# Kernel optimization log

Measured on AMD Instinct MI355X. Metric: run time of the kernel, lower is better.

## Reference

```python
import jax, jax.numpy as jnp
import numpy as np

N, D, H, K = 131072, 512, 128, 3
NPOS, NNEG = 8192, 8192
KM_ITERS = 4
PROTO_SHIFT = 0.15
PROTO_LOGIT_SCALE = 0.2
TEMP = 2.5


def _sq_cdist(x, c):
    # squared euclidean distance, matches torch.cdist(...).pow(2)
    d = jnp.sum(x * x, -1, keepdims=True) + jnp.sum(c * c, -1)[None, :] - 2.0 * (x @ c.T)
    return jnp.maximum(d, 0.0)


def _kmeans(x, k, iters):
    # torch.linspace(0, n-1, steps=k).long() init, fixed iteration count
    n = x.shape[0]
    idx = jnp.linspace(0.0, n - 1, k).astype(jnp.int32)
    centers = x[idx]
    for _ in range(iters):
        assign = jnp.argmin(_sq_cdist(x, centers), axis=1)
        sums = jax.ops.segment_sum(x, assign, num_segments=k)
        counts = jax.ops.segment_sum(jnp.ones((n,), x.dtype), assign, num_segments=k)[:, None]
        # empty cluster keeps old center (mask.any() branch in torch)
        centers = jnp.where(counts > 0, sums / jnp.maximum(counts, 1.0), centers)
    return centers


def setup_inputs() -> dict:
    key = jax.random.key(0)
    ks = jax.random.split(key, 10)
    s = 1.0 / np.sqrt(D).astype(np.float32)
    return {
        "z_cls": jax.random.normal(ks[0], (N, D), jnp.float32),
        "z_proto": jax.random.normal(ks[1], (N, D), jnp.float32),
        "pos_ctx": jax.random.normal(ks[2], (D,), jnp.float32),
        "neg_ctx": jax.random.normal(ks[3], (D,), jnp.float32),
        "W1": jax.random.normal(ks[4], (H, D), jnp.float32) * s,
        "b1": jnp.zeros((H,), jnp.float32),
        "W2": jax.random.normal(ks[5], (1, H), jnp.float32) * (1.0 / np.sqrt(H).astype(np.float32)),
        "b2": jnp.zeros((1,), jnp.float32),
        "Wp": jax.random.normal(ks[6], (D, D), jnp.float32) * s,
        "bp": jnp.zeros((D,), jnp.float32),
        "Wn": jax.random.normal(ks[7], (D, D), jnp.float32) * s,
        "bn": jnp.zeros((D,), jnp.float32),
        "pos_idx": jax.random.randint(ks[8], (NPOS,), 0, N),
        "neg_idx": jax.random.randint(ks[9], (NNEG,), 0, N),
    }


def reference(z_cls, z_proto, pos_ctx, neg_ctx, W1, b1, W2, b2, Wp, bp, Wn, bn, pos_idx, neg_idx):
    # _build_prototypes (pos_idx/neg_idx nonempty path)
    pos_proto = _kmeans(z_proto[pos_idx], K, KM_ITERS)          # [K, D]
    neg_proto = jnp.mean(z_proto[neg_idx], axis=0)              # [D]
    # _calibrate (ema not initialized -> no EMA blend)
    pos_proto = pos_proto + PROTO_SHIFT * (pos_ctx @ Wp.T + bp)[None, :]
    neg_proto = neg_proto + PROTO_SHIFT * (neg_ctx @ Wn.T + bn)
    # distances
    d_pos_all = _sq_cdist(z_proto, pos_proto)                   # [N, K]
    d_pos = jnp.min(d_pos_all, axis=1)
    pos_assign = jnp.argmin(d_pos_all, axis=1)
    d_neg = jnp.mean((z_proto - neg_proto[None, :]) ** 2, axis=1)
    proto_logit = (d_neg - d_pos) / np.sqrt(D).astype(np.float32)
    # cls head (eval mode: dropout is identity)
    h = jax.nn.relu(z_cls @ W1.T + b1)
    cls_logit = (h @ W2.T + b2)[:, 0]
    logits = (cls_logit + PROTO_LOGIT_SCALE * proto_logit) / TEMP
    prob = jax.nn.sigmoid(logits)
    return (logits, prob, PROTO_LOGIT_SCALE * proto_logit, pos_assign, d_pos_all, pos_proto, neg_proto)
```

## Files before the change

### kernel.cpp

```cpp
#include <hip/hip_runtime.h>
#include <hip/hip_bf16.h>

#define NPTS 131072
#define DIM  512
#define HID  128
#define KCL  3
#define NPOSI 8192
#define NNEGI 8192

typedef __attribute__((ext_vector_type(8))) short bf16x8;
typedef __attribute__((ext_vector_type(4))) float f32x4;

enum {
  WS_SHIFT_POS = 0,
  WS_SHIFT_NEG = 512,
  WS_NEGSUM    = 1024,
  WS_NEGPART   = 1536,
  WS_SUMS      = 67072,
  WS_W1FRAG    = 73232,
};
#define SUMS_STRIDE 1539

__device__ __forceinline__ short f2bf(float x) {
  __hip_bfloat16 h = __float2bfloat16(x);
  return *reinterpret_cast<short*>(&h);
}

__global__ __launch_bounds__(256) void k_prep(const float* __restrict__ W1,
                                              const float* __restrict__ Wp, const float* __restrict__ bp,
                                              const float* __restrict__ Wn, const float* __restrict__ bn,
                                              const float* __restrict__ pos_ctx, const float* __restrict__ neg_ctx,
                                              const float* __restrict__ zp, const int* __restrict__ neg_idx,
                                              float* __restrict__ ws) {
  int bid = blockIdx.x, t = threadIdx.x;
  if (bid < 32) {
    int fid = bid * 256 + t;
    int kc = fid >> 9;
    int n  = (fid >> 6) & 7;
    int l  = fid & 63;
    int row = n * 16 + (l & 15);
    int col = kc * 32 + (l >> 4) * 8;
    const float* src = W1 + (size_t)row * DIM + col;
    float4 v0 = *(const float4*)(src);
    float4 v1 = *(const float4*)(src + 4);
    bf16x8 f;
    f[0] = f2bf(v0.x); f[1] = f2bf(v0.y); f[2] = f2bf(v0.z); f[3] = f2bf(v0.w);
    f[4] = f2bf(v1.x); f[5] = f2bf(v1.y); f[6] = f2bf(v1.z); f[7] = f2bf(v1.w);
    ((bf16x8*)(ws + WS_W1FRAG))[fid] = f;
  } else if (bid < 64) {
    int b = bid - 32;
    int mat = b >> 4;
    const float* W    = mat ? Wn : Wp;
    const float* bias = mat ? bn : bp;
    const float* ctx  = mat ? neg_ctx : pos_ctx;
    float* outp = ws + (mat ? WS_SHIFT_NEG : WS_SHIFT_POS);
    int row = (b & 15) * 32 + (t >> 3);
    int sub = t & 7;
    const float* wr = W + row * DIM + sub * 64;
    const float* cr = ctx + sub * 64;
    float s = 0.f;
#pragma unroll
    for (int j = 0; j < 64; j += 4) {
      float4 w4 = *(const float4*)(wr + j);
      float4 c4 = *(const float4*)(cr + j);
      s += w4.x * c4.x + w4.y * c4.y + w4.z * c4.z + w4.w * c4.w;
    }
    s += __shfl_xor(s, 1);
    s += __shfl_xor(s, 2);
    s += __shfl_xor(s, 4);
    if (sub == 0) outp[row] = 0.15f * (s + bias[row]);
  } else if (bid < 192) {
    int j = bid - 64;
    int c0 = t * 2;
    float a0 = 0.f, a1 = 0.f;
    int j0 = j * 64;
    for (int jj = 0; jj < 64; ++jj) {
      int row = neg_idx[j0 + jj];
      float2 v = *(const float2*)(zp + (size_t)row * DIM + c0);
      a0 += v.x; a1 += v.y;
    }
    ws[WS_NEGPART + j * DIM + c0]     = a0;
    ws[WS_NEGPART + j * DIM + c0 + 1] = a1;
  } else {
    for (int idx = t; idx < 4 * SUMS_STRIDE; idx += 256) ws[WS_SUMS + idx] = 0.f;
  }
}

template <int IT>
__global__ __launch_bounds__(256) void k_km(const float* __restrict__ zp,
                                            const int* __restrict__ pos_idx,
                                            float* __restrict__ ws) {
  int bid = blockIdx.x, t = threadIdx.x;
  if (IT == 0 && bid == 256) {
    int c0 = t * 2;
    float a0 = 0.f, a1 = 0.f;
#pragma unroll 8
    for (int j = 0; j < 128; ++j) {
      float2 v = *(const float2*)(ws + WS_NEGPART + j * DIM + c0);
      a0 += v.x; a1 += v.y;
    }
    ws[WS_NEGSUM + c0]     = a0;
    ws[WS_NEGSUM + c0 + 1] = a1;
    return;
  }
  __shared__ float cc[KCL * DIM];
  __shared__ float cn[KCL];
  __shared__ float lsum[KCL * DIM];
  __shared__ float lcnt[KCL];
  int w = t >> 6, l = t & 63;

  for (int idx = t; idx < KCL * DIM; idx += 256) lsum[idx] = 0.f;
  if (t < KCL) lcnt[t] = 0.f;

  for (int idx = t; idx < KCL * DIM; idx += 256) {
    int k = idx >> 9;
    int sel = (k == 0) ? 0 : ((k == 1) ? 4095 : 8191);
    float v = zp[(size_t)pos_idx[sel] * DIM + (idx & 511)];
#pragma unroll
    for (int j = 0; j < IT; ++j) {
      float cntv = ws[WS_SUMS + j * SUMS_STRIDE + 3 * DIM + k];
      float sv   = ws[WS_SUMS + j * SUMS_STRIDE + idx];
      v = (cntv > 0.f) ? sv / cntv : v;
    }
    cc[idx] = v;
  }
  __syncthreads();
  if (w < KCL) {
    float s = 0.f;
#pragma unroll
    for (int m = 0; m < 8; ++m) { float v = cc[w * DIM + l + m * 64]; s += v * v; }
#pragma unroll
    for (int m = 1; m < 64; m <<= 1) s += __shfl_xor(s, m);
    if (l == 0) cn[w] = s;
  }
  __syncthreads();

  float ck0[8], ck1[8], ck2[8];
#pragma unroll
  for (int j = 0; j < 8; ++j) {
    ck0[j] = cc[0 * DIM + l * 8 + j];
    ck1[j] = cc[1 * DIM + l * 8 + j];
    ck2[j] = cc[2 * DIM + l * 8 + j];
  }
  float cn0 = cn[0], cn1 = cn[1], cn2 = cn[2];
  float acc0[8] = {0,0,0,0,0,0,0,0}, acc1[8] = {0,0,0,0,0,0,0,0}, acc2[8] = {0,0,0,0,0,0,0,0};
  float cnt0 = 0.f, cnt1 = 0.f, cnt2 = 0.f;

  int wid = bid * 4 + w;
  for (int p = wid; p < NPOSI; p += 1024) {
    int row = pos_idx[p];
    const float* xr = zp + (size_t)row * DIM + l * 8;
    float4 x0 = *(const float4*)(xr);
    float4 x1 = *(const float4*)(xr + 4);
    float x[8] = {x0.x, x0.y, x0.z, x0.w, x1.x, x1.y, x1.z, x1.w};
    float d0 = 0.f, d1 = 0.f, d2 = 0.f;
#pragma unroll
    for (int j = 0; j < 8; ++j) { d0 += x[j] * ck0[j]; d1 += x[j] * ck1[j]; d2 += x[j] * ck2[j]; }
#pragma unroll
    for (int m = 1; m < 64; m <<= 1) {
      d0 += __shfl_xor(d0, m); d1 += __shfl_xor(d1, m); d2 += __shfl_xor(d2, m);
    }
    float t0 = cn0 - 2.f * d0, t1 = cn1 - 2.f * d1, t2 = cn2 - 2.f * d2;
    int a = 0; float best = t0;
    if (t1 < best) { best = t1; a = 1; }
    if (t2 < best) { best = t2; a = 2; }
    if (a == 0)      { cnt0 += 1.f;
#pragma unroll
      for (int j = 0; j < 8; ++j) acc0[j] += x[j]; }
    else if (a == 1) { cnt1 += 1.f;
#pragma unroll
      for (int j = 0; j < 8; ++j) acc1[j] += x[j]; }
    else             { cnt2 += 1.f;
#pragma unroll
      for (int j = 0; j < 8; ++j) acc2[j] += x[j]; }
  }
#pragma unroll
  for (int j = 0; j < 8; ++j) {
    atomicAdd(&lsum[0 * DIM + l * 8 + j], acc0[j]);
    atomicAdd(&lsum[1 * DIM + l * 8 + j], acc1[j]);
    atomicAdd(&lsum[2 * DIM + l * 8 + j], acc2[j]);
  }
  if (l == 0) {
    atomicAdd(&lcnt[0], cnt0); atomicAdd(&lcnt[1], cnt1); atomicAdd(&lcnt[2], cnt2);
  }
  __syncthreads();
  for (int idx = t; idx < KCL * DIM; idx += 256) atomicAdd(&ws[WS_SUMS + IT * SUMS_STRIDE + idx], lsum[idx]);
  if (t < KCL) atomicAdd(&ws[WS_SUMS + IT * SUMS_STRIDE + 3 * DIM + t], lcnt[t]);
}

__global__ __launch_bounds__(256) void k_main(const float* __restrict__ zc,
                                              const float* __restrict__ zp,
                                              const float* __restrict__ b1,
                                              const float* __restrict__ W2,
                                              const float* __restrict__ b2,
                                              const int* __restrict__ pos_idx,
                                              const float* __restrict__ ws,
                                              float* __restrict__ out) {
  __shared__ float pp[KCL * DIM];
  __shared__ float np[DIM];
  __shared__ float pn[4];
  __shared__ float clsv[64];
  __shared__ float sxs[64];
  __shared__ float dstg[4][64];
  __shared__ float outst[448];
  __shared__ bf16x8 pfrag[1024];

  int t = threadIdx.x, w = t >> 6, l = t & 63;
  int i0 = blockIdx.x * 64;

  for (int idx = t; idx < KCL * DIM; idx += 256) {
    int k = idx >> 9, d = idx & 511;
    int sel = (k == 0) ? 0 : ((k == 1) ? 4095 : 8191);
    float v = zp[(size_t)pos_idx[sel] * DIM + d];
#pragma unroll
    for (int j = 0; j < 4; ++j) {
      float cntv = ws[WS_SUMS + j * SUMS_STRIDE + 3 * DIM + k];
      float sv   = ws[WS_SUMS + j * SUMS_STRIDE + idx];
      v = (cntv > 0.f) ? sv / cntv : v;
    }
    pp[idx] = v + ws[WS_SHIFT_POS + d];
  }
  for (int d = t; d < DIM; d += 256)
    np[d] = ws[WS_NEGSUM + d] * (1.f / NNEGI) + ws[WS_SHIFT_NEG + d];
  __syncthreads();
  {
    float s = 0.f;
    const float* src = (w < 3) ? (pp + w * DIM) : np;
#pragma unroll
    for (int m = 0; m < 8; ++m) { float v = src[l + m * 64]; s += v * v; }
#pragma unroll
    for (int m = 1; m < 64; m <<= 1) s += __shfl_xor(s, m);
    if (l == 0) pn[w] = s;
  }
  for (int idx = t; idx < 1024; idx += 256) {
    int kc = idx >> 6, ll = idx & 63, c = ll & 15, ko = (ll >> 4) * 8;
    bf16x8 v;
#pragma unroll
    for (int j = 0; j < 8; ++j) {
      float f = (c < 3) ? pp[c * DIM + kc * 32 + ko + j]
                        : ((c == 3) ? np[kc * 32 + ko + j] : 0.f);
      v[j] = f2bf(f);
    }
    pfrag[idx] = v;
  }
  if (blockIdx.x == 0) {
    for (int idx = t; idx < KCL * DIM; idx += 256) out[7 * NPTS + idx] = pp[idx];
    for (int d = t; d < DIM; d += 256)            out[7 * NPTS + KCL * DIM + d] = np[d];
  }
  __syncthreads();

  const bf16x8* w1f = (const bf16x8*)(ws + WS_W1FRAG);
  int arow = i0 + w * 16 + (l & 15);
  const float* zcrow = zc + (size_t)arow * DIM + (l >> 4) * 8;
  const float* zprow = zp + (size_t)arow * DIM + (l >> 4) * 8;

  f32x4 accc[8];
#pragma unroll
  for (int n = 0; n < 8; ++n) accc[n] = (f32x4){0.f, 0.f, 0.f, 0.f};
  f32x4 accd = (f32x4){0.f, 0.f, 0.f, 0.f};
  float sx = 0.f;

  for (int kc = 0; kc < 16; ++kc) {
    float4 c0 = *(const float4*)(zcrow + kc * 32);
    float4 c1 = *(const float4*)(zcrow + kc * 32 + 4);
    float4 p0 = *(const float4*)(zprow + kc * 32);
    float4 p1 = *(const float4*)(zprow + kc * 32 + 4);
    bf16x8 af, ap;
    af[0] = f2bf(c0.x); af[1] = f2bf(c0.y); af[2] = f2bf(c0.z); af[3] = f2bf(c0.w);
    af[4] = f2bf(c1.x); af[5] = f2bf(c1.y); af[6] = f2bf(c1.z); af[7] = f2bf(c1.w);
    ap[0] = f2bf(p0.x); ap[1] = f2bf(p0.y); ap[2] = f2bf(p0.z); ap[3] = f2bf(p0.w);
    ap[4] = f2bf(p1.x); ap[5] = f2bf(p1.y); ap[6] = f2bf(p1.z); ap[7] = f2bf(p1.w);
    sx += p0.x * p0.x + p0.y * p0.y + p0.z * p0.z + p0.w * p0.w
        + p1.x * p1.x + p1.y * p1.y + p1.z * p1.z + p1.w * p1.w;
    accd = __builtin_amdgcn_mfma_f32_16x16x32_bf16(ap, pfrag[kc * 64 + l], accd, 0, 0, 0);
    const bf16x8* wrow = w1f + kc * 512 + l;
#pragma unroll
    for (int n = 0; n < 8; ++n)
      accc[n] = __builtin_amdgcn_mfma_f32_16x16x32_bf16(af, wrow[n * 64], accc[n], 0, 0, 0);
  }

  sx += __shfl_xor(sx, 16);
  sx += __shfl_xor(sx, 32);
  if (l < 16) sxs[w * 16 + l] = sx;

  {
    float pcl[4] = {0.f, 0.f, 0.f, 0.f};
    int col_l = l & 15;
#pragma unroll
    for (int n = 0; n < 8; ++n) {
      int col = n * 16 + col_l;
      float bb = b1[col], w2v = W2[col];
#pragma unroll
      for (int r = 0; r < 4; ++r) {
        float h = accc[n][r] + bb;
        h = h > 0.f ? h : 0.f;
        pcl[r] += h * w2v;
      }
    }
#pragma unroll
    for (int m = 1; m < 16; m <<= 1) {
#pragma unroll
      for (int r = 0; r < 4; ++r) pcl[r] += __shfl_xor(pcl[r], m);
    }
    if (col_l == 0) {
      float b2v = b2[0];
#pragma unroll
      for (int r = 0; r < 4; ++r) clsv[w * 16 + (l >> 4) * 4 + r] = pcl[r] + b2v;
    }
  }
  {
    int c = l & 15;
    if (c < 4) {
#pragma unroll
      for (int j = 0; j < 4; ++j) dstg[c][w * 16 + (l >> 4) * 4 + j] = accd[j];
    }
  }
  __syncthreads();

  if (t < 64) {
    float sxv = sxs[t];
    float d0 = dstg[0][t], d1 = dstg[1][t], d2 = dstg[2][t], dn = dstg[3][t];
    float e0 = sxv + pn[0] - 2.f * d0; e0 = fmaxf(e0, 0.f);
    float e1 = sxv + pn[1] - 2.f * d1; e1 = fmaxf(e1, 0.f);
    float e2 = sxv + pn[2] - 2.f * d2; e2 = fmaxf(e2, 0.f);
    float dpos = e0; int a = 0;
    if (e1 < dpos) { dpos = e1; a = 1; }
    if (e2 < dpos) { dpos = e2; a = 2; }
    float dneg = (sxv + pn[3] - 2.f * dn) * (1.f / DIM);
    float plog = (dneg - dpos) * 0.04419417382415922f;
    float o2 = 0.2f * plog;
    float lg = (clsv[t] + o2) * 0.4f;
    float prob = 1.f / (1.f + expf(-lg));
    outst[t]        = lg;
    outst[64 + t]   = prob;
    outst[128 + t]  = o2;
    outst[192 + t]  = (float)a;
    outst[256 + 3 * t]     = e0;
    outst[256 + 3 * t + 1] = e1;
    outst[256 + 3 * t + 2] = e2;
  }
  __syncthreads();
  if (t < 64) {
    out[i0 + t]            = outst[t];
    out[NPTS + i0 + t]     = outst[64 + t];
    out[2 * NPTS + i0 + t] = outst[128 + t];
    out[3 * NPTS + i0 + t] = outst[192 + t];
  } else {
    int u = t - 64;
    if (u < 192) out[4 * NPTS + 3 * i0 + u] = outst[256 + u];
  }
}

extern "C" void kernel_launch(void* const* d_in, const int* in_sizes, int n_in,
                              void* d_out, int out_size, void* d_ws, size_t ws_size,
                              hipStream_t stream) {
  const float* z_cls   = (const float*)d_in[0];
  const float* z_proto = (const float*)d_in[1];
  const float* pos_ctx = (const float*)d_in[2];
  const float* neg_ctx = (const float*)d_in[3];
  const float* W1      = (const float*)d_in[4];
  const float* b1      = (const float*)d_in[5];
  const float* W2      = (const float*)d_in[6];
  const float* b2      = (const float*)d_in[7];
  const float* Wp      = (const float*)d_in[8];
  const float* bp      = (const float*)d_in[9];
  const float* Wn      = (const float*)d_in[10];
  const float* bn      = (const float*)d_in[11];
  const int* pos_idx   = (const int*)d_in[12];
  const int* neg_idx   = (const int*)d_in[13];
  float* out           = (float*)d_out;
  float* ws            = (float*)d_ws;

  k_prep<<<193, 256, 0, stream>>>(W1, Wp, bp, Wn, bn, pos_ctx, neg_ctx, z_proto, neg_idx, ws);
  k_km<0><<<257, 256, 0, stream>>>(z_proto, pos_idx, ws);
  k_km<1><<<256, 256, 0, stream>>>(z_proto, pos_idx, ws);
  k_km<2><<<256, 256, 0, stream>>>(z_proto, pos_idx, ws);
  k_km<3><<<256, 256, 0, stream>>>(z_proto, pos_idx, ws);
  k_main<<<NPTS / 64, 256, 0, stream>>>(z_cls, z_proto, b1, W2, b2, pos_idx, ws, out);
}
```

Before: 289.9 us.

## Split main kernel into cls MFMA, proto-distance fp32, and finalize kernels

Breaks the fused main kernel into three kernels. A single-block finalize computes the prototypes and their norms once. An MFMA classifier kernel software-pipelines its z_cls and W1 fragment loads and writes cls logits to the workspace. A separate fp32 kernel computes the prototype distances and all outputs. The negative-mean gather is also spread over twice as many blocks, and the k-means loop gets an unroll hint. The split drops per-block prototype rebuilding and the bf16 packing of prototypes, and computes the distances in fp32. In exchange it adds two launches and an extra workspace round trip for the cls logits.

```diff
diff --git a/kernel.cpp b/kernel.cpp
--- a/kernel.cpp
+++ b/kernel.cpp
@@ -16,8 +16,11 @@
   WS_SHIFT_NEG = 512,
   WS_NEGSUM    = 1024,
   WS_NEGPART   = 1536,
-  WS_SUMS      = 67072,
-  WS_W1FRAG    = 73232,
+  WS_SUMS      = 132608,
+  WS_PPROTO    = 138764,
+  WS_PN        = 140812,
+  WS_W1FRAG    = 140816,
+  WS_CLSL      = 173584,
 };
 #define SUMS_STRIDE 1539
 
@@ -69,18 +72,19 @@
     s += __shfl_xor(s, 2);
     s += __shfl_xor(s, 4);
     if (sub == 0) outp[row] = 0.15f * (s + bias[row]);
-  } else if (bid < 192) {
-    int j = bid - 64;
+  } else if (bid < 320) {
+    int jb = bid - 64;
     int c0 = t * 2;
     float a0 = 0.f, a1 = 0.f;
-    int j0 = j * 64;
-    for (int jj = 0; jj < 64; ++jj) {
-      int row = neg_idx[j0 + jj];
+    int base = jb * 32;
+#pragma unroll 4
+    for (int jj = 0; jj < 32; ++jj) {
+      int row = neg_idx[base + jj];
       float2 v = *(const float2*)(zp + (size_t)row * DIM + c0);
       a0 += v.x; a1 += v.y;
     }
-    ws[WS_NEGPART + j * DIM + c0]     = a0;
-    ws[WS_NEGPART + j * DIM + c0 + 1] = a1;
+    ws[WS_NEGPART + jb * DIM + c0]     = a0;
+    ws[WS_NEGPART + jb * DIM + c0 + 1] = a1;
   } else {
     for (int idx = t; idx < 4 * SUMS_STRIDE; idx += 256) ws[WS_SUMS + idx] = 0.f;
   }
@@ -95,7 +99,7 @@
     int c0 = t * 2;
     float a0 = 0.f, a1 = 0.f;
 #pragma unroll 8
-    for (int j = 0; j < 128; ++j) {
+    for (int j = 0; j < 256; ++j) {
       float2 v = *(const float2*)(ws + WS_NEGPART + j * DIM + c0);
       a0 += v.x; a1 += v.y;
     }
@@ -147,6 +151,7 @@
   float cnt0 = 0.f, cnt1 = 0.f, cnt2 = 0.f;
 
   int wid = bid * 4 + w;
+#pragma unroll 2
   for (int p = wid; p < NPOSI; p += 1024) {
     int row = pos_idx[p];
     const float* xr = zp + (size_t)row * DIM + l * 8;
@@ -188,26 +193,12 @@
   if (t < KCL) atomicAdd(&ws[WS_SUMS + IT * SUMS_STRIDE + 3 * DIM + t], lcnt[t]);
 }
 
-__global__ __launch_bounds__(256) void k_main(const float* __restrict__ zc,
-                                              const float* __restrict__ zp,
-                                              const float* __restrict__ b1,
-                                              const float* __restrict__ W2,
-                                              const float* __restrict__ b2,
-                                              const int* __restrict__ pos_idx,
-                                              const float* __restrict__ ws,
-                                              float* __restrict__ out) {
-  __shared__ float pp[KCL * DIM];
-  __shared__ float np[DIM];
-  __shared__ float pn[4];
-  __shared__ float clsv[64];
-  __shared__ float sxs[64];
-  __shared__ float dstg[4][64];
-  __shared__ float outst[448];
-  __shared__ bf16x8 pfrag[1024];
-
+__global__ __launch_bounds__(256) void k_fin(const float* __restrict__ zp,
+                                             const int* __restrict__ pos_idx,
+                                             float* __restrict__ ws,
+                                             float* __restrict__ out) {
+  __shared__ __align__(16) float pp[4 * DIM];
   int t = threadIdx.x, w = t >> 6, l = t & 63;
-  int i0 = blockIdx.x * 64;
-
   for (int idx = t; idx < KCL * DIM; idx += 256) {
     int k = idx >> 9, d = idx & 511;
     int sel = (k == 0) ? 0 : ((k == 1) ? 4095 : 8191);
@@ -221,133 +212,148 @@
     pp[idx] = v + ws[WS_SHIFT_POS + d];
   }
   for (int d = t; d < DIM; d += 256)
-    np[d] = ws[WS_NEGSUM + d] * (1.f / NNEGI) + ws[WS_SHIFT_NEG + d];
+    pp[3 * DIM + d] = ws[WS_NEGSUM + d] * (1.f / NNEGI) + ws[WS_SHIFT_NEG + d];
   __syncthreads();
   {
     float s = 0.f;
-    const float* src = (w < 3) ? (pp + w * DIM) : np;
-#pragma unroll
-    for (int m = 0; m < 8; ++m) { float v = src[l + m * 64]; s += v * v; }
+#pragma unroll
+    for (int m = 0; m < 8; ++m) { float v = pp[w * DIM + l + m * 64]; s += v * v; }
 #pragma unroll
     for (int m = 1; m < 64; m <<= 1) s += __shfl_xor(s, m);
-    if (l == 0) pn[w] = s;
-  }
-  for (int idx = t; idx < 1024; idx += 256) {
-    int kc = idx >> 6, ll = idx & 63, c = ll & 15, ko = (ll >> 4) * 8;
-    bf16x8 v;
-#pragma unroll
-    for (int j = 0; j < 8; ++j) {
-      float f = (c < 3) ? pp[c * DIM + kc * 32 + ko + j]
-                        : ((c == 3) ? np[kc * 32 + ko + j] : 0.f);
-      v[j] = f2bf(f);
-    }
-    pfrag[idx] = v;
-  }
-  if (blockIdx.x == 0) {
-    for (int idx = t; idx < KCL * DIM; idx += 256) out[7 * NPTS + idx] = pp[idx];
-    for (int d = t; d < DIM; d += 256)            out[7 * NPTS + KCL * DIM + d] = np[d];
-  }
-  __syncthreads();
-
+    if (l == 0) ws[WS_PN + w] = s;
+  }
+  for (int idx = t; idx < 4 * DIM; idx += 256) {
+    ws[WS_PPROTO + idx] = pp[idx];
+    out[7 * NPTS + idx] = pp[idx];
+  }
+}
+
+__global__ __launch_bounds__(256, 2) void k_cls(const float* __restrict__ zc,
+                                                const float* __restrict__ b1,
+                                                const float* __restrict__ W2,
+                                                const float* __restrict__ b2,
+                                                float* __restrict__ ws) {
+  int t = threadIdx.x, w = t >> 6, l = t & 63;
+  int i0 = blockIdx.x * 64;
   const bf16x8* w1f = (const bf16x8*)(ws + WS_W1FRAG);
   int arow = i0 + w * 16 + (l & 15);
-  const float* zcrow = zc + (size_t)arow * DIM + (l >> 4) * 8;
-  const float* zprow = zp + (size_t)arow * DIM + (l >> 4) * 8;
-
-  f32x4 accc[8];
-#pragma unroll
-  for (int n = 0; n < 8; ++n) accc[n] = (f32x4){0.f, 0.f, 0.f, 0.f};
-  f32x4 accd = (f32x4){0.f, 0.f, 0.f, 0.f};
-  float sx = 0.f;
-
+  const float* aptr = zc + (size_t)arow * DIM + (l >> 4) * 8;
+
+  f32x4 acc[8];
+#pragma unroll
+  for (int n = 0; n < 8; ++n) acc[n] = (f32x4){0.f, 0.f, 0.f, 0.f};
+
+  float4 A[3][2];
+  bf16x8 B[2][8];
+#pragma unroll
+  for (int s = 0; s < 3; ++s) {
+    A[s][0] = *(const float4*)(aptr + s * 32);
+    A[s][1] = *(const float4*)(aptr + s * 32 + 4);
+  }
+#pragma unroll
+  for (int n = 0; n < 8; ++n) B[0][n] = w1f[n * 64 + l];
+
+#pragma unroll
   for (int kc = 0; kc < 16; ++kc) {
-    float4 c0 = *(const float4*)(zcrow + kc * 32);
-    float4 c1 = *(const float4*)(zcrow + kc * 32 + 4);
-    float4 p0 = *(const float4*)(zprow + kc * 32);
-    float4 p1 = *(const float4*)(zprow + kc * 32 + 4);
-    bf16x8 af, ap;
-    af[0] = f2bf(c0.x); af[1] = f2bf(c0.y); af[2] = f2bf(c0.z); af[3] = f2bf(c0.w);
-    af[4] = f2bf(c1.x); af[5] = f2bf(c1.y); af[6] = f2bf(c1.z); af[7] = f2bf(c1.w);
-    ap[0] = f2bf(p0.x); ap[1] = f2bf(p0.y); ap[2] = f2bf(p0.z); ap[3] = f2bf(p0.w);
-    ap[4] = f2bf(p1.x); ap[5] = f2bf(p1.y); ap[6] = f2bf(p1.z); ap[7] = f2bf(p1.w);
-    sx += p0.x * p0.x + p0.y * p0.y + p0.z * p0.z + p0.w * p0.w
-        + p1.x * p1.x + p1.y * p1.y + p1.z * p1.z + p1.w * p1.w;
-    accd = __builtin_amdgcn_mfma_f32_16x16x32_bf16(ap, pfrag[kc * 64 + l], accd, 0, 0, 0);
-    const bf16x8* wrow = w1f + kc * 512 + l;
+    float4 a0 = A[kc % 3][0], a1 = A[kc % 3][1];
+    bf16x8 af;
+    af[0] = f2bf(a0.x); af[1] = f2bf(a0.y); af[2] = f2bf(a0.z); af[3] = f2bf(a0.w);
+    af[4] = f2bf(a1.x); af[5] = f2bf(a1.y); af[6] = f2bf(a1.z); af[7] = f2bf(a1.w);
+    if (kc + 3 < 16) {
+      A[kc % 3][0] = *(const float4*)(aptr + (kc + 3) * 32);
+      A[kc % 3][1] = *(const float4*)(aptr + (kc + 3) * 32 + 4);
+    }
+    if (kc + 1 < 16) {
+#pragma unroll
+      for (int n = 0; n < 8; ++n) B[(kc + 1) & 1][n] = w1f[(kc + 1) * 512 + n * 64 + l];
+    }
 #pragma unroll
     for (int n = 0; n < 8; ++n)
-      accc[n] = __builtin_amdgcn_mfma_f32_16x16x32_bf16(af, wrow[n * 64], accc[n], 0, 0, 0);
-  }
-
-  sx += __shfl_xor(sx, 16);
-  sx += __shfl_xor(sx, 32);
-  if (l < 16) sxs[w * 16 + l] = sx;
-
-  {
-    float pcl[4] = {0.f, 0.f, 0.f, 0.f};
-    int col_l = l & 15;
-#pragma unroll
-    for (int n = 0; n < 8; ++n) {
-      int col = n * 16 + col_l;
-      float bb = b1[col], w2v = W2[col];
-#pragma unroll
-      for (int r = 0; r < 4; ++r) {
-        float h = accc[n][r] + bb;
-        h = h > 0.f ? h : 0.f;
-        pcl[r] += h * w2v;
-      }
-    }
-#pragma unroll
-    for (int m = 1; m < 16; m <<= 1) {
-#pragma unroll
-      for (int r = 0; r < 4; ++r) pcl[r] += __shfl_xor(pcl[r], m);
-    }
-    if (col_l == 0) {
-      float b2v = b2[0];
-#pragma unroll
-      for (int r = 0; r < 4; ++r) clsv[w * 16 + (l >> 4) * 4 + r] = pcl[r] + b2v;
-    }
-  }
-  {
-    int c = l & 15;
-    if (c < 4) {
-#pragma unroll
-      for (int j = 0; j < 4; ++j) dstg[c][w * 16 + (l >> 4) * 4 + j] = accd[j];
-    }
-  }
-  __syncthreads();
-
-  if (t < 64) {
-    float sxv = sxs[t];
-    float d0 = dstg[0][t], d1 = dstg[1][t], d2 = dstg[2][t], dn = dstg[3][t];
-    float e0 = sxv + pn[0] - 2.f * d0; e0 = fmaxf(e0, 0.f);
-    float e1 = sxv + pn[1] - 2.f * d1; e1 = fmaxf(e1, 0.f);
-    float e2 = sxv + pn[2] - 2.f * d2; e2 = fmaxf(e2, 0.f);
+      acc[n] = __builtin_amdgcn_mfma_f32_16x16x32_bf16(af, B[kc & 1][n], acc[n], 0, 0, 0);
+  }
+
+  float p[4] = {0.f, 0.f, 0.f, 0.f};
+  int col_l = l & 15;
+#pragma unroll
+  for (int n = 0; n < 8; ++n) {
+    int col = n * 16 + col_l;
+    float bb = b1[col], w2v = W2[col];
+#pragma unroll
+    for (int r = 0; r < 4; ++r) {
+      float h = acc[n][r] + bb;
+      h = h > 0.f ? h : 0.f;
+      p[r] += h * w2v;
+    }
+  }
+#pragma unroll
+  for (int m = 1; m < 16; m <<= 1) {
+#pragma unroll
+    for (int r = 0; r < 4; ++r) p[r] += __shfl_xor(p[r], m);
+  }
+  if (col_l == 0) {
+    float b2v = b2[0];
+    int rbase = i0 + w * 16 + (l >> 4) * 4;
+#pragma unroll
+    for (int r = 0; r < 4; ++r) ws[WS_CLSL + rbase + r] = p[r] + b2v;
+  }
+}
+
+__global__ __launch_bounds__(256, 4) void k_proto(const float* __restrict__ zp,
+                                                  const float* __restrict__ ws,
+                                                  float* __restrict__ out) {
+  __shared__ __align__(16) float pp[4 * DIM];
+  __shared__ float pns[4];
+  int t = threadIdx.x;
+  for (int idx = t; idx < 4 * DIM; idx += 256) pp[idx] = ws[WS_PPROTO + idx];
+  if (t < 4) pns[t] = ws[WS_PN + t];
+  __syncthreads();
+
+  int w = t >> 6, l = t & 63, s = l & 7, r = l >> 3;
+  int i = blockIdx.x * 32 + w * 8 + r;
+  const float* xr = zp + (size_t)i * DIM;
+
+  float d0 = 0.f, d1 = 0.f, d2 = 0.f, dn = 0.f, sx = 0.f;
+#pragma unroll
+  for (int j = 0; j < 16; ++j) {
+    int col = j * 32 + s * 4;
+    float4 x  = *(const float4*)(xr + col);
+    float4 c0 = *(const float4*)(&pp[0 * DIM + col]);
+    float4 c1 = *(const float4*)(&pp[1 * DIM + col]);
+    float4 c2 = *(const float4*)(&pp[2 * DIM + col]);
+    float4 c3 = *(const float4*)(&pp[3 * DIM + col]);
+    d0 += x.x * c0.x + x.y * c0.y + x.z * c0.z + x.w * c0.w;
+    d1 += x.x * c1.x + x.y * c1.y + x.z * c1.z + x.w * c1.w;
+    d2 += x.x * c2.x + x.y * c2.y + x.z * c2.z + x.w * c2.w;
+    dn += x.x * c3.x + x.y * c3.y + x.z * c3.z + x.w * c3.w;
+    sx += x.x * x.x  + x.y * x.y  + x.z * x.z  + x.w * x.w;
+  }
+#pragma unroll
+  for (int m = 1; m < 8; m <<= 1) {
+    d0 += __shfl_xor(d0, m);
+    d1 += __shfl_xor(d1, m);
+    d2 += __shfl_xor(d2, m);
+    dn += __shfl_xor(dn, m);
+    sx += __shfl_xor(sx, m);
+  }
+  if (s == 0) {
+    float e0 = sx + pns[0] - 2.f * d0; e0 = fmaxf(e0, 0.f);
+    float e1 = sx + pns[1] - 2.f * d1; e1 = fmaxf(e1, 0.f);
+    float e2 = sx + pns[2] - 2.f * d2; e2 = fmaxf(e2, 0.f);
     float dpos = e0; int a = 0;
     if (e1 < dpos) { dpos = e1; a = 1; }
     if (e2 < dpos) { dpos = e2; a = 2; }
-    float dneg = (sxv + pn[3] - 2.f * dn) * (1.f / DIM);
+    float dneg = (sx + pns[3] - 2.f * dn) * (1.f / DIM);
     float plog = (dneg - dpos) * 0.04419417382415922f;
     float o2 = 0.2f * plog;
-    float lg = (clsv[t] + o2) * 0.4f;
+    float lg = (ws[WS_CLSL + i] + o2) * 0.4f;
     float prob = 1.f / (1.f + expf(-lg));
-    outst[t]        = lg;
-    outst[64 + t]   = prob;
-    outst[128 + t]  = o2;
-    outst[192 + t]  = (float)a;
-    outst[256 + 3 * t]     = e0;
-    outst[256 + 3 * t + 1] = e1;
-    outst[256 + 3 * t + 2] = e2;
-  }
-  __syncthreads();
-  if (t < 64) {
-    out[i0 + t]            = outst[t];
-    out[NPTS + i0 + t]     = outst[64 + t];
-    out[2 * NPTS + i0 + t] = outst[128 + t];
-    out[3 * NPTS + i0 + t] = outst[192 + t];
-  } else {
-    int u = t - 64;
-    if (u < 192) out[4 * NPTS + 3 * i0 + u] = outst[256 + u];
+    out[i]            = lg;
+    out[NPTS + i]     = prob;
+    out[2 * NPTS + i] = o2;
+    out[3 * NPTS + i] = (float)a;
+    out[4 * NPTS + 3 * i]     = e0;
+    out[4 * NPTS + 3 * i + 1] = e1;
+    out[4 * NPTS + 3 * i + 2] = e2;
   }
 }
 
@@ -371,10 +377,12 @@
   float* out           = (float*)d_out;
   float* ws            = (float*)d_ws;
 
-  k_prep<<<193, 256, 0, stream>>>(W1, Wp, bp, Wn, bn, pos_ctx, neg_ctx, z_proto, neg_idx, ws);
+  k_prep<<<321, 256, 0, stream>>>(W1, Wp, bp, Wn, bn, pos_ctx, neg_ctx, z_proto, neg_idx, ws);
   k_km<0><<<257, 256, 0, stream>>>(z_proto, pos_idx, ws);
   k_km<1><<<256, 256, 0, stream>>>(z_proto, pos_idx, ws);
   k_km<2><<<256, 256, 0, stream>>>(z_proto, pos_idx, ws);
   k_km<3><<<256, 256, 0, stream>>>(z_proto, pos_idx, ws);
-  k_main<<<NPTS / 64, 256, 0, stream>>>(z_cls, z_proto, b1, W2, b2, pos_idx, ws, out);
-}
+  k_fin<<<1, 256, 0, stream>>>(z_proto, pos_idx, ws, out);
+  k_cls<<<NPTS / 64, 256, 0, stream>>>(z_cls, b1, W2, b2, ws);
+  k_proto<<<NPTS / 32, 256, 0, stream>>>(z_proto, ws, out);
+}
```

After: 276.1 us. 4.8% less time.
